# Performance work log

Measured on AMD Instinct MI355X. Metric: run time of the kernel, lower is better.

The kernel has to match this reference:

```python
import jax, jax.numpy as jnp
import numpy as np

# Module hyperparameters (init_kwargs)
NUM_EXPERTS = 8
HIDDEN = 1024
CAP_FACTORS = [0.5, 0.75, 1.0, 1.0, 1.25, 1.25, 1.5, 1.5]


def setup_inputs() -> dict:
    key = jax.random.key(0)
    k1, k2, k3 = jax.random.split(key, 3)
    G, T = 4, 2048
    token_inputs = jax.random.normal(k1, (G, T, HIDDEN), dtype=jnp.float32)
    # RouterWeights = nn.Linear(hidden, num_experts, bias=True)
    W = jax.random.normal(k2, (HIDDEN, NUM_EXPERTS), dtype=jnp.float32) * (1.0 / np.sqrt(HIDDEN))
    b = jax.random.normal(k3, (NUM_EXPERTS,), dtype=jnp.float32) * 0.01
    return {"token_inputs": token_inputs, "W": W, "b": b, "expert_capacity": 256}


def reference(token_inputs, W, b, expert_capacity):
    # token_inputs: [G, T, H]; jitter_noise=0 so no jitter; ignore_padding_tokens=False
    G, T, _ = token_inputs.shape
    logits = jnp.einsum("gth,he->gte", token_inputs, W) + b  # [G, T, E]
    probs = jax.nn.softmax(logits, axis=-1)
    # router z-loss: mean(logsumexp(logits, -1)^2)
    z_loss = jnp.mean(jax.nn.logsumexp(logits, axis=-1) ** 2)

    capacities = [int(expert_capacity * f) for f in CAP_FACTORS]
    max_cap = max(capacities)

    dispatch_slices = []  # each [G, T, max_cap] int32
    combine_slices = []   # each [G, T, max_cap] float32
    for e, cap in enumerate(capacities):
        gate, idx = jax.lax.top_k(probs[:, :, e], cap)  # [G, cap]
        # one_hot(idx, T): [G, cap, T] -> transpose to [G, T, cap]
        oh = jax.nn.one_hot(idx, T, dtype=jnp.int32).transpose(0, 2, 1)  # [G, T, cap]
        oh = jnp.pad(oh, ((0, 0), (0, 0), (0, max_cap - cap)))
        dispatch_slices.append(oh)
        # combine: gate broadcast over tokens dim (as in original code)
        comb = jnp.broadcast_to(gate[:, None, :], (G, T, cap))  # [G, T, cap]
        comb = jnp.pad(comb, ((0, 0), (0, 0), (0, max_cap - cap)))
        combine_slices.append(comb)

    dispatch_mask = jnp.stack(dispatch_slices, axis=1)  # [G, E, T, max_cap]
    combine_array = jnp.stack(combine_slices, axis=1).astype(jnp.float32)  # [G, E, T, max_cap]
    auxiliary_loss = jnp.float32(0.0)
    return dispatch_mask, combine_array, auxiliary_loss, z_loss
```

## Files before the change

### kernel.cpp

```cpp
#include <hip/hip_runtime.h>
#include <hip/hip_bf16.h>
#include <math.h>

#define G 4
#define T 2048
#define H 1024
#define E 8
#define NBUK 2048
#define K1B 2048
#define K2B 256

typedef float f4 __attribute__((ext_vector_type(4)));
typedef unsigned long long u64;

__global__ __launch_bounds__(256) void k1_zero_logits(
    const float* __restrict__ x, const float* __restrict__ W,
    const float* __restrict__ b, u64* __restrict__ keys,
    float* __restrict__ lse2, float* __restrict__ out, unsigned n4d) {
  unsigned bid = blockIdx.x;
  unsigned tid = threadIdx.x;

  {
    f4* outD = (f4*)out;
    f4 z = {0.0f, 0.0f, 0.0f, 0.0f};
    for (unsigned i = bid * 256u + tid; i < n4d; i += K1B * 256u) outD[i] = z;
  }

  int wave = (int)(bid * 4 + (tid >> 6));
  int lane = (int)(tid & 63);
  const float* xr = x + (size_t)wave * H;

  double acc0 = 0, acc1 = 0, acc2 = 0, acc3 = 0;
  double acc4 = 0, acc5 = 0, acc6 = 0, acc7 = 0;
#pragma unroll
  for (int j = 0; j < 4; ++j) {
    int hbase = j * 256 + lane * 4;
    f4 xv = *(const f4*)(xr + hbase);
#pragma unroll
    for (int k = 0; k < 4; ++k) {
      const float* wr = W + (size_t)(hbase + k) * 8;
      f4 w0 = *(const f4*)(wr);
      f4 w1 = *(const f4*)(wr + 4);
      double xd = (double)xv[k];
      acc0 += xd * (double)w0[0];
      acc1 += xd * (double)w0[1];
      acc2 += xd * (double)w0[2];
      acc3 += xd * (double)w0[3];
      acc4 += xd * (double)w1[0];
      acc5 += xd * (double)w1[1];
      acc6 += xd * (double)w1[2];
      acc7 += xd * (double)w1[3];
    }
  }
#pragma unroll
  for (int off = 32; off >= 1; off >>= 1) {
    acc0 += __shfl_xor(acc0, off);
    acc1 += __shfl_xor(acc1, off);
    acc2 += __shfl_xor(acc2, off);
    acc3 += __shfl_xor(acc3, off);
    acc4 += __shfl_xor(acc4, off);
    acc5 += __shfl_xor(acc5, off);
    acc6 += __shfl_xor(acc6, off);
    acc7 += __shfl_xor(acc7, off);
  }
  double l0 = acc0 + (double)b[0], l1 = acc1 + (double)b[1];
  double l2 = acc2 + (double)b[2], l3 = acc3 + (double)b[3];
  double l4 = acc4 + (double)b[4], l5 = acc5 + (double)b[5];
  double l6 = acc6 + (double)b[6], l7 = acc7 + (double)b[7];
  double m = fmax(fmax(fmax(l0, l1), fmax(l2, l3)),
                  fmax(fmax(l4, l5), fmax(l6, l7)));
  double la = (lane & 1) ? l1 : l0;
  double lb = (lane & 1) ? l3 : l2;
  double lc = (lane & 1) ? l5 : l4;
  double ld = (lane & 1) ? l7 : l6;
  double le = (lane & 2) ? lb : la;
  double lf = (lane & 2) ? ld : lc;
  double lsel = (lane & 4) ? lf : le;

  double pe = exp(lsel - m);
  double s = pe;
  s += __shfl_xor(s, 1);
  s += __shfl_xor(s, 2);
  s += __shfl_xor(s, 4);
  double inv = 1.0 / s;
  float pf = (float)(pe * inv);

  int g = wave >> 11;
  int t = wave & (T - 1);
  if (lane < 8) {
    keys[((size_t)g * 8 + lane) * T + t] =
        ((u64)__float_as_uint(pf) << 32) | (unsigned)(~t);
  }
  if (lane == 0) {
    double lse = m + log(s);
    lse2[wave] = (float)(lse * lse);
  }
}

__global__ __launch_bounds__(1024) void k2_select_combine(
    const u64* __restrict__ keys, const float* __restrict__ lse2,
    float* __restrict__ out, unsigned n4d, int max_cap, int ec) {
  __shared__ int hist[NBUK];
  __shared__ int sA[NBUK];
  __shared__ int sB[NBUK];
  __shared__ int cur[NBUK];
  __shared__ u64 srt[T];
  __shared__ float gLds[1024];
  __shared__ double red[256];

  unsigned bid = blockIdx.x;
  unsigned tid = threadIdx.x;
  unsigned mc = (unsigned)max_cap;
  unsigned mc4 = mc >> 2;
  int ge = (int)(bid >> 3);
  int sl = (int)(bid & 7);

  hist[tid] = 0;
  hist[tid + 1024] = 0;
  if (tid < mc) gLds[tid] = 0.0f;
  __syncthreads();

  const u64* kcol = keys + (size_t)ge * T;
  u64 k0 = kcol[tid];
  u64 k1 = kcol[tid + 1024];
  int b0 = (int)(k0 >> 53);
  int b1 = (int)(k1 >> 53);
  atomicAdd(&hist[b0], 1);
  atomicAdd(&hist[b1], 1);
  __syncthreads();

  sA[tid] = hist[tid];
  sA[tid + 1024] = hist[tid + 1024];
  __syncthreads();
  int* src = sA;
  int* dst = sB;
  for (int s = 1; s < NBUK; s <<= 1) {
    for (int i = (int)tid; i < NBUK; i += 1024) {
      int v = src[i];
      if (i + s < NBUK) v += src[i + s];
      dst[i] = v;
    }
    __syncthreads();
    int* tmp = src;
    src = dst;
    dst = tmp;
  }
  for (int i = (int)tid; i < NBUK; i += 1024) cur[i] = src[i] - hist[i];
  __syncthreads();

  int p0 = atomicAdd(&cur[b0], 1);
  srt[p0] = k0;
  int p1 = atomicAdd(&cur[b1], 1);
  srt[p1] = k1;
  __syncthreads();

  const double factors[8] = {0.5, 0.75, 1.0, 1.0, 1.25, 1.25, 1.5, 1.5};
  int cap = (int)((double)ec * factors[ge & 7]);

  int o0 = src[b0] - hist[b0];
  if (o0 < cap) {
    int end = src[b0];
    int c = 0;
    for (int i = o0; i < end; ++i) c += (int)(srt[i] > k0);
    int r = o0 + c;
    if (r < cap) {
      unsigned t = ~(unsigned)k0;
      gLds[r] = __uint_as_float((unsigned)(k0 >> 32));
      out[((size_t)ge * T + t) * mc + r] = 1.0f;
    }
  }
  int o1 = src[b1] - hist[b1];
  if (o1 < cap) {
    int end = src[b1];
    int c = 0;
    for (int i = o1; i < end; ++i) c += (int)(srt[i] > k1);
    int r = o1 + c;
    if (r < cap) {
      unsigned t = ~(unsigned)k1;
      gLds[r] = __uint_as_float((unsigned)(k1 >> 32));
      out[((size_t)ge * T + t) * mc + r] = 1.0f;
    }
  }
  __syncthreads();

  {
    const f4* gl4 = (const f4*)gLds;
    unsigned rows = T / 8;
    unsigned slabf4 = rows * mc4;
    f4* dstC = (f4*)out + n4d + ((size_t)ge * T + (unsigned)sl * rows) * mc4;
    unsigned c4 = tid % mc4;
    unsigned step = 1024u % mc4;
    for (unsigned i = tid; i < slabf4; i += 1024u) {
      dstC[i] = gl4[c4];
      c4 += step;
      if (c4 >= mc4) c4 -= mc4;
    }
  }

  if (bid == 0) {
    if (tid < 256) {
      double s = 0.0;
      for (int i = (int)tid; i < G * T; i += 256) s += (double)lse2[i];
      red[tid] = s;
    }
    __syncthreads();
    for (int off = 128; off > 0; off >>= 1) {
      if ((int)tid < off) red[tid] += red[tid + off];
      __syncthreads();
    }
    if (tid == 0) {
      size_t ne = (size_t)n4d * 4;
      out[2 * ne] = 0.0f;
      out[2 * ne + 1] = (float)(red[0] / (double)(G * T));
    }
  }
}

extern "C" void kernel_launch(void* const* d_in, const int* in_sizes, int n_in,
                              void* d_out, int out_size, void* d_ws,
                              size_t ws_size, hipStream_t stream) {
  const float* x = (const float*)d_in[0];
  const float* W = (const float*)d_in[1];
  const float* b = (const float*)d_in[2];

  long long body = (long long)out_size - 2;
  int max_cap = (int)(body / (2LL * G * E * T));
  if (max_cap <= 0) return;
  int ec = (2 * max_cap) / 3;

  u64* keys = (u64*)d_ws;
  float* lse2 = (float*)(keys + (size_t)G * E * T);

  unsigned n4d = (unsigned)((long long)G * E * T * max_cap / 4);

  k1_zero_logits<<<K1B, 256, 0, stream>>>(x, W, b, keys, lse2, (float*)d_out,
                                          n4d);
  k2_select_combine<<<K2B, 1024, 0, stream>>>(keys, lse2, (float*)d_out, n4d,
                                              max_cap, ec);
}
```

Baseline: 73.89 us.

## Write dispatch mask densely in select kernel instead of zero-fill plus scatter

The dispatch mask is no longer zero-filled by the logits kernel and then patched with scattered ones. Instead the select kernel records each token's rank in shared memory and writes its slab of the dispatch mask in one pass, emitting full float4 rows of zeros and ones. This removes the separate zero-fill from the first kernel and replaces the scattered single-float stores with coalesced vector stores. A template specialisation for max_cap 384 makes the per-row division by mc4 a compile-time constant. The cost is that the dense write now lands entirely in the 256-block second kernel, so it no longer overlaps with the logits work.

```diff
diff --git a/kernel.cpp b/kernel.cpp
--- a/kernel.cpp
+++ b/kernel.cpp
@@ -13,21 +13,12 @@
 typedef float f4 __attribute__((ext_vector_type(4)));
 typedef unsigned long long u64;
 
-__global__ __launch_bounds__(256) void k1_zero_logits(
+__global__ __launch_bounds__(256) void k1_logits(
     const float* __restrict__ x, const float* __restrict__ W,
     const float* __restrict__ b, u64* __restrict__ keys,
-    float* __restrict__ lse2, float* __restrict__ out, unsigned n4d) {
-  unsigned bid = blockIdx.x;
-  unsigned tid = threadIdx.x;
-
-  {
-    f4* outD = (f4*)out;
-    f4 z = {0.0f, 0.0f, 0.0f, 0.0f};
-    for (unsigned i = bid * 256u + tid; i < n4d; i += K1B * 256u) outD[i] = z;
-  }
-
-  int wave = (int)(bid * 4 + (tid >> 6));
-  int lane = (int)(tid & 63);
+    float* __restrict__ lse2) {
+  int wave = (int)(blockIdx.x * 4 + (threadIdx.x >> 6));
+  int lane = (int)(threadIdx.x & 63);
   const float* xr = x + (size_t)wave * H;
 
   double acc0 = 0, acc1 = 0, acc2 = 0, acc3 = 0;
@@ -97,21 +88,24 @@
   }
 }
 
-__global__ __launch_bounds__(1024) void k2_select_combine(
+template <int MC4S>
+__global__ __launch_bounds__(1024) void k2_select_write(
     const u64* __restrict__ keys, const float* __restrict__ lse2,
-    float* __restrict__ out, unsigned n4d, int max_cap, int ec) {
+    float* __restrict__ out, unsigned n4d, int max_cap, int ec,
+    unsigned mc4_rt) {
   __shared__ int hist[NBUK];
   __shared__ int sA[NBUK];
   __shared__ int sB[NBUK];
   __shared__ int cur[NBUK];
   __shared__ u64 srt[T];
   __shared__ float gLds[1024];
+  __shared__ int rankLds[T];
   __shared__ double red[256];
 
+  const unsigned mc4 = MC4S ? (unsigned)MC4S : mc4_rt;
   unsigned bid = blockIdx.x;
   unsigned tid = threadIdx.x;
   unsigned mc = (unsigned)max_cap;
-  unsigned mc4 = mc >> 2;
   int ge = (int)(bid >> 3);
   int sl = (int)(bid & 7);
 
@@ -157,6 +151,7 @@
   const double factors[8] = {0.5, 0.75, 1.0, 1.0, 1.25, 1.25, 1.5, 1.5};
   int cap = (int)((double)ec * factors[ge & 7]);
 
+  int rk0 = -1, rk1 = -1;
   int o0 = src[b0] - hist[b0];
   if (o0 < cap) {
     int end = src[b0];
@@ -164,9 +159,8 @@
     for (int i = o0; i < end; ++i) c += (int)(srt[i] > k0);
     int r = o0 + c;
     if (r < cap) {
-      unsigned t = ~(unsigned)k0;
+      rk0 = r;
       gLds[r] = __uint_as_float((unsigned)(k0 >> 32));
-      out[((size_t)ge * T + t) * mc + r] = 1.0f;
     }
   }
   int o1 = src[b1] - hist[b1];
@@ -176,17 +170,35 @@
     for (int i = o1; i < end; ++i) c += (int)(srt[i] > k1);
     int r = o1 + c;
     if (r < cap) {
-      unsigned t = ~(unsigned)k1;
+      rk1 = r;
       gLds[r] = __uint_as_float((unsigned)(k1 >> 32));
-      out[((size_t)ge * T + t) * mc + r] = 1.0f;
-    }
-  }
-  __syncthreads();
+    }
+  }
+  rankLds[tid] = rk0;
+  rankLds[tid + 1024] = rk1;
+  __syncthreads();
+
+  unsigned rows = T / 8;
+  unsigned slabf4 = rows * mc4;
+
+  {
+    f4* dstD = (f4*)out + ((size_t)ge * T + (unsigned)sl * rows) * mc4;
+    for (unsigned i = tid; i < slabf4; i += 1024u) {
+      unsigned row = i / mc4;
+      unsigned c4 = i - row * mc4;
+      int r = rankLds[sl * (int)rows + (int)row];
+      int base = (int)(c4 * 4);
+      f4 dv;
+      dv.x = (r == base) ? 1.0f : 0.0f;
+      dv.y = (r == base + 1) ? 1.0f : 0.0f;
+      dv.z = (r == base + 2) ? 1.0f : 0.0f;
+      dv.w = (r == base + 3) ? 1.0f : 0.0f;
+      dstD[i] = dv;
+    }
+  }
 
   {
     const f4* gl4 = (const f4*)gLds;
-    unsigned rows = T / 8;
-    unsigned slabf4 = rows * mc4;
     f4* dstC = (f4*)out + n4d + ((size_t)ge * T + (unsigned)sl * rows) * mc4;
     unsigned c4 = tid % mc4;
     unsigned step = 1024u % mc4;
@@ -233,8 +245,12 @@
 
   unsigned n4d = (unsigned)((long long)G * E * T * max_cap / 4);
 
-  k1_zero_logits<<<K1B, 256, 0, stream>>>(x, W, b, keys, lse2, (float*)d_out,
-                                          n4d);
-  k2_select_combine<<<K2B, 1024, 0, stream>>>(keys, lse2, (float*)d_out, n4d,
-                                              max_cap, ec);
+  k1_logits<<<K1B, 256, 0, stream>>>(x, W, b, keys, lse2);
+  if (max_cap == 384) {
+    k2_select_write<96><<<K2B, 1024, 0, stream>>>(keys, lse2, (float*)d_out,
+                                                  n4d, max_cap, ec, 96u);
+  } else {
+    k2_select_write<0><<<K2B, 1024, 0, stream>>>(
+        keys, lse2, (float*)d_out, n4d, max_cap, ec, (unsigned)(max_cap / 4));
+  }
 }
```

Result: slower. 82.54 us (+11.7%).

## Split selection and combine broadcast into separate kernels with a wide combine grid

Applied to the files above, without the earlier changes.

Before, each group/expert top-k selection was repeated eight times, once per block slice that also wrote a slab of the combine array. Now one block per group/expert does the selection and writes gates to workspace. A new 2048-block kernel then broadcasts gates across the whole combine array and also computes z-loss. This removes the 8x redundant sorting work and spreads the large combine write over many more blocks, at the cost of an extra launch and a global round-trip for the gates. A template specialization makes the column divide a compile-time constant for the default capacity.

```diff
diff --git a/kernel.cpp b/kernel.cpp
--- a/kernel.cpp
+++ b/kernel.cpp
@@ -8,7 +8,7 @@
 #define E 8
 #define NBUK 2048
 #define K1B 2048
-#define K2B 256
+#define K3B 2048
 
 typedef float f4 __attribute__((ext_vector_type(4)));
 typedef unsigned long long u64;
@@ -97,27 +97,22 @@
   }
 }
 
-__global__ __launch_bounds__(1024) void k2_select_combine(
-    const u64* __restrict__ keys, const float* __restrict__ lse2,
-    float* __restrict__ out, unsigned n4d, int max_cap, int ec) {
+__global__ __launch_bounds__(1024) void k2_select(
+    const u64* __restrict__ keys, float* __restrict__ gate,
+    float* __restrict__ out, int max_cap, int ec) {
   __shared__ int hist[NBUK];
   __shared__ int sA[NBUK];
   __shared__ int sB[NBUK];
   __shared__ int cur[NBUK];
   __shared__ u64 srt[T];
-  __shared__ float gLds[1024];
-  __shared__ double red[256];
-
-  unsigned bid = blockIdx.x;
+
   unsigned tid = threadIdx.x;
   unsigned mc = (unsigned)max_cap;
-  unsigned mc4 = mc >> 2;
-  int ge = (int)(bid >> 3);
-  int sl = (int)(bid & 7);
+  int ge = (int)blockIdx.x;
 
   hist[tid] = 0;
   hist[tid + 1024] = 0;
-  if (tid < mc) gLds[tid] = 0.0f;
+  if (tid < mc) gate[(size_t)ge * mc + tid] = 0.0f;
   __syncthreads();
 
   const u64* kcol = keys + (size_t)ge * T;
@@ -165,7 +160,7 @@
     int r = o0 + c;
     if (r < cap) {
       unsigned t = ~(unsigned)k0;
-      gLds[r] = __uint_as_float((unsigned)(k0 >> 32));
+      gate[(size_t)ge * mc + r] = __uint_as_float((unsigned)(k0 >> 32));
       out[((size_t)ge * T + t) * mc + r] = 1.0f;
     }
   }
@@ -177,32 +172,25 @@
     int r = o1 + c;
     if (r < cap) {
       unsigned t = ~(unsigned)k1;
-      gLds[r] = __uint_as_float((unsigned)(k1 >> 32));
+      gate[(size_t)ge * mc + r] = __uint_as_float((unsigned)(k1 >> 32));
       out[((size_t)ge * T + t) * mc + r] = 1.0f;
     }
   }
-  __syncthreads();
-
-  {
-    const f4* gl4 = (const f4*)gLds;
-    unsigned rows = T / 8;
-    unsigned slabf4 = rows * mc4;
-    f4* dstC = (f4*)out + n4d + ((size_t)ge * T + (unsigned)sl * rows) * mc4;
-    unsigned c4 = tid % mc4;
-    unsigned step = 1024u % mc4;
-    for (unsigned i = tid; i < slabf4; i += 1024u) {
-      dstC[i] = gl4[c4];
-      c4 += step;
-      if (c4 >= mc4) c4 -= mc4;
-    }
-  }
+}
+
+template <int MC4S>
+__global__ __launch_bounds__(256) void k3_combine(
+    const float* __restrict__ gate, const float* __restrict__ lse2,
+    float* __restrict__ out, unsigned n4d, unsigned mc4_rt) {
+  const unsigned mc4 = MC4S ? (unsigned)MC4S : mc4_rt;
+  unsigned tid = threadIdx.x;
+  unsigned bid = blockIdx.x;
 
   if (bid == 0) {
-    if (tid < 256) {
-      double s = 0.0;
-      for (int i = (int)tid; i < G * T; i += 256) s += (double)lse2[i];
-      red[tid] = s;
-    }
+    __shared__ double red[256];
+    double s = 0.0;
+    for (int i = (int)tid; i < G * T; i += 256) s += (double)lse2[i];
+    red[tid] = s;
     __syncthreads();
     for (int off = 128; off > 0; off >>= 1) {
       if ((int)tid < off) red[tid] += red[tid + off];
@@ -213,6 +201,18 @@
       out[2 * ne] = 0.0f;
       out[2 * ne + 1] = (float)(red[0] / (double)(G * T));
     }
+    return;
+  }
+
+  f4* outC = (f4*)out + n4d;
+  const f4* gate4 = (const f4*)gate;
+  unsigned fb = bid - 1;
+  unsigned stride = (K3B - 1) * 256u;
+  for (unsigned i = fb * 256u + tid; i < n4d; i += stride) {
+    unsigned row = i / mc4;
+    unsigned c4 = i - row * mc4;
+    unsigned ge = row >> 11;
+    outC[i] = gate4[ge * mc4 + c4];
   }
 }
 
@@ -230,11 +230,19 @@
 
   u64* keys = (u64*)d_ws;
   float* lse2 = (float*)(keys + (size_t)G * E * T);
+  float* gate = lse2 + (size_t)G * T;
 
   unsigned n4d = (unsigned)((long long)G * E * T * max_cap / 4);
 
   k1_zero_logits<<<K1B, 256, 0, stream>>>(x, W, b, keys, lse2, (float*)d_out,
                                           n4d);
-  k2_select_combine<<<K2B, 1024, 0, stream>>>(keys, lse2, (float*)d_out, n4d,
-                                              max_cap, ec);
-}
+  k2_select<<<G * E, 1024, 0, stream>>>(keys, gate, (float*)d_out, max_cap,
+                                        ec);
+  if (max_cap == 384) {
+    k3_combine<96><<<K3B, 256, 0, stream>>>(gate, lse2, (float*)d_out, n4d,
+                                            96u);
+  } else {
+    k3_combine<0><<<K3B, 256, 0, stream>>>(gate, lse2, (float*)d_out, n4d,
+                                           (unsigned)(max_cap / 4));
+  }
+}
```

After: 80.10 us. 8.4% more time.
